# Performance work log

Measured on AMD Instinct MI355X. Metric: run time of the kernel, lower is better.

## Reference

```python
import jax, jax.numpy as jnp
import numpy as np

NEG_INF_FILL = -1000000.0  # matches torch code's masked fill value


def setup_inputs() -> dict:
    key = jax.random.key(0)
    kK, kV, kQ, kL = jax.random.split(key, 4)
    B, Sq, Sk, d, dv = 8, 2048, 2048, 512, 512
    return {
        "K": jax.random.normal(kK, (B, Sk, d), dtype=jnp.float32),
        "V": jax.random.normal(kV, (B, Sk, dv), dtype=jnp.float32),
        "Q": jax.random.normal(kQ, (B, Sq, d), dtype=jnp.float32),
        "valid_len": jax.random.randint(kL, (Sq,), 0, dv, dtype=jnp.int64),
    }


def reference(K, V, Q, valid_len):
    d = K.shape[-1]
    # score: [B, Sq, Sk]
    score = jnp.einsum("bqd,bkd->bqk", Q, K) / jnp.sqrt(jnp.asarray(d, Q.dtype))
    # x: [B, Sq, dv] -- NOTE: original applies mask+softmax to score @ V
    x = jnp.einsum("bqk,bkv->bqv", score, V)
    dv = x.shape[-1]
    # mask rows: per-query-position valid_len compared to feature index 0..dv-1
    mask = jnp.arange(dv)[None, :] > valid_len[:, None]  # [Sq, dv]
    x = jnp.where(mask[None, :, :], jnp.asarray(NEG_INF_FILL, x.dtype), x)
    return jax.nn.softmax(x, axis=-1)
```

## Files before the change

### kernel.cpp

```cpp
#include <hip/hip_runtime.h>
#include <hip/hip_bf16.h>
#include <math.h>

#define BATCH 8
#define SQ 2048
#define SK 2048
#define DD 512
#define DV 512
#define RP 40

typedef short bf16x8_t __attribute__((ext_vector_type(8)));
typedef float f32x4_t __attribute__((ext_vector_type(4)));

__device__ __forceinline__ unsigned int pk_bf16(float a, float b) {
    __hip_bfloat162 h = __float22bfloat162_rn(float2{a, b});
    unsigned int u;
    __builtin_memcpy(&u, &h, 4);
    return u;
}
__device__ __forceinline__ float from_hi(unsigned int u) {
    return __builtin_bit_cast(float, u);
}

__global__ __launch_bounds__(256) void ktv_mfma(const float* __restrict__ Kp,
                                                const float* __restrict__ Vp,
                                                float* __restrict__ Mpart) {
    const int b  = blockIdx.z & 7;
    const int ts = blockIdx.z >> 3;
    const int d0 = blockIdx.x * 128;
    const int v0 = blockIdx.y * 128;
    const float* Kb = Kp + (size_t)b * SK * DD;
    const float* Vb = Vp + (size_t)b * SK * DV;

    __shared__ __align__(16) unsigned short Kh[128 * RP], Kl[128 * RP],
                                            Vh[128 * RP], Vl[128 * RP];

    const int tid  = threadIdx.x;
    const int lane = tid & 63;
    const int w    = tid >> 6;
    const int wd   = (w & 1) * 64;
    const int wv   = (w >> 1) * 64;
    const int uu   = tid >> 5;
    const int xx   = tid & 31;

    f32x4_t acc[4][4];
#pragma unroll
    for (int i = 0; i < 4; ++i)
#pragma unroll
        for (int j = 0; j < 4; ++j) acc[i][j] = (f32x4_t){0.f, 0.f, 0.f, 0.f};

    const int tb = ts * 512;

    float kr0[2][4], kr1[2][4], vr0[2][4], vr1[2][4];
    auto load_tile = [&](int t0l) {
#pragma unroll
        for (int p = 0; p < 2; ++p) {
            const int t = 16 * p + 2 * uu;
            const size_t gr = (size_t)(tb + t0l + t);
#pragma unroll
            for (int c = 0; c < 4; ++c) {
                const int d = xx + 32 * c;
                kr0[p][c] = Kb[gr * DD + d0 + d];
                kr1[p][c] = Kb[(gr + 1) * DD + d0 + d];
                vr0[p][c] = Vb[gr * DV + v0 + d];
                vr1[p][c] = Vb[(gr + 1) * DV + v0 + d];
            }
        }
    };

    load_tile(0);
    for (int t0 = 0; t0 < 512; t0 += 32) {
#pragma unroll
        for (int p = 0; p < 2; ++p) {
            const int t  = 16 * p + 2 * uu;
            const int to = (t >> 3) * 8 + (t & 7);
#pragma unroll
            for (int c = 0; c < 4; ++c) {
                const int d   = xx + 32 * c;
                const int off = d * RP + to;
                {
                    const unsigned int h = pk_bf16(kr0[p][c], kr1[p][c]);
                    const float r0 = kr0[p][c] - from_hi(h << 16);
                    const float r1 = kr1[p][c] - from_hi(h & 0xFFFF0000u);
                    *(unsigned int*)(Kh + off) = h;
                    *(unsigned int*)(Kl + off) = pk_bf16(r0, r1);
                }
                {
                    const unsigned int h = pk_bf16(vr0[p][c], vr1[p][c]);
                    const float r0 = vr0[p][c] - from_hi(h << 16);
                    const float r1 = vr1[p][c] - from_hi(h & 0xFFFF0000u);
                    *(unsigned int*)(Vh + off) = h;
                    *(unsigned int*)(Vl + off) = pk_bf16(r0, r1);
                }
            }
        }
        __syncthreads();

        if (t0 + 32 < 512) load_tile(t0 + 32);

        const int kq = lane >> 4;
        const int mr = lane & 15;
        bf16x8_t ah[4], al_[4];
#pragma unroll
        for (int tm = 0; tm < 4; ++tm) {
            const int off = (wd + tm * 16 + mr) * RP + kq * 8;
            ah[tm]  = *(const bf16x8_t*)(Kh + off);
            al_[tm] = *(const bf16x8_t*)(Kl + off);
        }
#pragma unroll
        for (int tn = 0; tn < 4; ++tn) {
            const int off = (wv + tn * 16 + mr) * RP + kq * 8;
            const bf16x8_t bh = *(const bf16x8_t*)(Vh + off);
            const bf16x8_t bl = *(const bf16x8_t*)(Vl + off);
#pragma unroll
            for (int tm = 0; tm < 4; ++tm) {
                acc[tm][tn] = __builtin_amdgcn_mfma_f32_16x16x32_bf16(ah[tm], bh, acc[tm][tn], 0, 0, 0);
                acc[tm][tn] = __builtin_amdgcn_mfma_f32_16x16x32_bf16(ah[tm], bl, acc[tm][tn], 0, 0, 0);
                acc[tm][tn] = __builtin_amdgcn_mfma_f32_16x16x32_bf16(al_[tm], bh, acc[tm][tn], 0, 0, 0);
            }
        }
        __syncthreads();
    }

    float* Mp = Mpart + (size_t)(ts * 8 + b) * DD * DV;
    const int quad = lane >> 4;
    const int col  = lane & 15;
#pragma unroll
    for (int tm = 0; tm < 4; ++tm)
#pragma unroll
        for (int tn = 0; tn < 4; ++tn)
#pragma unroll
            for (int r = 0; r < 4; ++r) {
                const int d = d0 + wd + tm * 16 + quad * 4 + r;
                const int v = v0 + wv + tn * 16 + col;
                Mp[(size_t)d * DV + v] = acc[tm][tn][r];
            }
}

__global__ __launch_bounds__(256) void reduce_cvt(const float* __restrict__ Mpart,
                                                  unsigned short* __restrict__ Mth,
                                                  unsigned short* __restrict__ Mtl) {
    const int b  = blockIdx.z;
    const int d0 = blockIdx.x * 64;
    const int v0 = blockIdx.y * 64;
    __shared__ float T[64][65];
    const int i  = threadIdx.x;
    const int xr = i >> 4;
    const int xc = i & 15;

#pragma unroll
    for (int e = 0; e < 4; ++e) {
        const int dr = e * 16 + xr;
        float sx = 0.f, sy = 0.f, sz = 0.f, sw = 0.f;
#pragma unroll
        for (int sl = 0; sl < 4; ++sl) {
            const float4 f = *(const float4*)&Mpart[((size_t)(sl * 8 + b) * DD + d0 + dr) * DV + v0 + xc * 4];
            sx += f.x; sy += f.y; sz += f.z; sw += f.w;
        }
        T[dr][xc * 4 + 0] = sx;
        T[dr][xc * 4 + 1] = sy;
        T[dr][xc * 4 + 2] = sz;
        T[dr][xc * 4 + 3] = sw;
    }
    __syncthreads();

    const float s = 0.04419417382415922f;
#pragma unroll
    for (int e = 0; e < 4; ++e) {
        const int v = e * 16 + xr;
        float m[4], r[4];
        unsigned int hv[2], lv[2];
#pragma unroll
        for (int j = 0; j < 4; ++j) m[j] = T[xc * 4 + j][v] * s;
#pragma unroll
        for (int j = 0; j < 2; ++j) {
            hv[j] = pk_bf16(m[2 * j], m[2 * j + 1]);
            r[2 * j]     = m[2 * j]     - from_hi(hv[j] << 16);
            r[2 * j + 1] = m[2 * j + 1] - from_hi(hv[j] & 0xFFFF0000u);
            lv[j] = pk_bf16(r[2 * j], r[2 * j + 1]);
        }
        const size_t o = ((size_t)b * DV + v0 + v) * DD + d0 + xc * 4;
        *(uint2*)&Mth[o] = make_uint2(hv[0], hv[1]);
        *(uint2*)&Mtl[o] = make_uint2(lv[0], lv[1]);
    }
}

__global__ __launch_bounds__(256) void qm_mfma(const float* __restrict__ Qp,
                                               const unsigned short* __restrict__ Mth,
                                               const unsigned short* __restrict__ Mtl,
                                               float* __restrict__ Xp) {
    const int b  = blockIdx.z;
    const int q0 = blockIdx.x * 128;
    const int v0 = blockIdx.y * 128;
    const float* Qb = Qp + (size_t)b * SQ * DD;
    const unsigned short* Bhg = Mth + (size_t)b * DV * DD;
    const unsigned short* Blg = Mtl + (size_t)b * DV * DD;

    __shared__ __align__(16) unsigned short Qh[128 * RP], Ql[128 * RP],
                                            Bh[128 * RP], Bl[128 * RP];

    const int tid  = threadIdx.x;
    const int lane = tid & 63;
    const int w    = tid >> 6;
    const int wq   = (w & 1) * 64;
    const int wv   = (w >> 1) * 64;

    f32x4_t acc[4][4];
#pragma unroll
    for (int i = 0; i < 4; ++i)
#pragma unroll
        for (int j = 0; j < 4; ++j) acc[i][j] = (f32x4_t){0.f, 0.f, 0.f, 0.f};

    float4 pq[4];
    bf16x8_t pbh[2], pbl[2];
    const int qrow = tid >> 3;
    const int qdc  = (tid & 7) * 4;
    const int brow = tid >> 2;
    const int bkq  = tid & 3;
    auto load_tile = [&](int k0l) {
#pragma unroll
        for (int p = 0; p < 4; ++p)
            pq[p] = *(const float4*)&Qb[(size_t)(q0 + p * 32 + qrow) * DD + k0l + qdc];
#pragma unroll
        for (int p = 0; p < 2; ++p) {
            const size_t go = (size_t)(v0 + p * 64 + brow) * DD + k0l + bkq * 8;
            pbh[p] = *(const bf16x8_t*)&Bhg[go];
            pbl[p] = *(const bf16x8_t*)&Blg[go];
        }
    };

    load_tile(0);
    for (int k0 = 0; k0 < DD; k0 += 32) {
#pragma unroll
        for (int p = 0; p < 4; ++p) {
            const float4 f = pq[p];
            const unsigned int h01 = pk_bf16(f.x, f.y);
            const unsigned int h23 = pk_bf16(f.z, f.w);
            const float r0 = f.x - from_hi(h01 << 16);
            const float r1 = f.y - from_hi(h01 & 0xFFFF0000u);
            const float r2 = f.z - from_hi(h23 << 16);
            const float r3 = f.w - from_hi(h23 & 0xFFFF0000u);
            const int off = (p * 32 + qrow) * RP + qdc;
            *(uint2*)(Qh + off) = make_uint2(h01, h23);
            *(uint2*)(Ql + off) = make_uint2(pk_bf16(r0, r1), pk_bf16(r2, r3));
        }
#pragma unroll
        for (int p = 0; p < 2; ++p) {
            const int off = (p * 64 + brow) * RP + bkq * 8;
            *(bf16x8_t*)(Bh + off) = pbh[p];
            *(bf16x8_t*)(Bl + off) = pbl[p];
        }
        __syncthreads();

        if (k0 + 32 < DD) load_tile(k0 + 32);

        const int kq = lane >> 4;
        const int mr = lane & 15;
        bf16x8_t ah[4], al_[4];
#pragma unroll
        for (int tm = 0; tm < 4; ++tm) {
            const int off = (wq + tm * 16 + mr) * RP + kq * 8;
            ah[tm]  = *(const bf16x8_t*)(Qh + off);
            al_[tm] = *(const bf16x8_t*)(Ql + off);
        }
#pragma unroll
        for (int tn = 0; tn < 4; ++tn) {
            const int off = (wv + tn * 16 + mr) * RP + kq * 8;
            const bf16x8_t bh = *(const bf16x8_t*)(Bh + off);
            const bf16x8_t bl = *(const bf16x8_t*)(Bl + off);
#pragma unroll
            for (int tm = 0; tm < 4; ++tm) {
                acc[tm][tn] = __builtin_amdgcn_mfma_f32_16x16x32_bf16(ah[tm], bh, acc[tm][tn], 0, 0, 0);
                acc[tm][tn] = __builtin_amdgcn_mfma_f32_16x16x32_bf16(ah[tm], bl, acc[tm][tn], 0, 0, 0);
                acc[tm][tn] = __builtin_amdgcn_mfma_f32_16x16x32_bf16(al_[tm], bh, acc[tm][tn], 0, 0, 0);
            }
        }
        __syncthreads();
    }

    float* Xb = Xp + (size_t)b * SQ * DV;
    const int quad = lane >> 4;
    const int col  = lane & 15;
#pragma unroll
    for (int tm = 0; tm < 4; ++tm)
#pragma unroll
        for (int tn = 0; tn < 4; ++tn)
#pragma unroll
            for (int r = 0; r < 4; ++r)
                Xb[(size_t)(q0 + wq + tm * 16 + quad * 4 + r) * DV + v0 + wv + tn * 16 + col] = acc[tm][tn][r];
}

__global__ __launch_bounds__(256) void softmax_kernel(float* __restrict__ X,
                                                      const int* __restrict__ vlen) {
    const int wave = threadIdx.x >> 6;
    const int lane = threadIdx.x & 63;
    const int row  = blockIdx.x * 4 + wave;
    const int q    = row & (SQ - 1);
    float* xr = X + (size_t)row * DV;
    const int vl = vlen[q];

    float v[8];
#pragma unroll
    for (int u = 0; u < 2; ++u) {
        const int j0 = u * 256 + lane * 4;
        const float4 f = *(const float4*)&xr[j0];
        v[u * 4 + 0] = (j0 + 0 > vl) ? -1.0e6f : f.x;
        v[u * 4 + 1] = (j0 + 1 > vl) ? -1.0e6f : f.y;
        v[u * 4 + 2] = (j0 + 2 > vl) ? -1.0e6f : f.z;
        v[u * 4 + 3] = (j0 + 3 > vl) ? -1.0e6f : f.w;
    }

    float m = v[0];
#pragma unroll
    for (int i = 1; i < 8; ++i) m = fmaxf(m, v[i]);
#pragma unroll
    for (int off = 32; off > 0; off >>= 1) m = fmaxf(m, __shfl_xor(m, off, 64));

    float ssum = 0.f;
#pragma unroll
    for (int i = 0; i < 8; ++i) {
        v[i] = __expf(v[i] - m);
        ssum += v[i];
    }
#pragma unroll
    for (int off = 32; off > 0; off >>= 1) ssum += __shfl_xor(ssum, off, 64);

    const float inv = 1.0f / ssum;
#pragma unroll
    for (int u = 0; u < 2; ++u) {
        const int j0 = u * 256 + lane * 4;
        float4 o;
        o.x = v[u * 4 + 0] * inv;
        o.y = v[u * 4 + 1] * inv;
        o.z = v[u * 4 + 2] * inv;
        o.w = v[u * 4 + 3] * inv;
        *(float4*)&xr[j0] = o;
    }
}

extern "C" void kernel_launch(void* const* d_in, const int* in_sizes, int n_in,
                              void* d_out, int out_size, void* d_ws, size_t ws_size,
                              hipStream_t stream) {
    const float* Kp   = (const float*)d_in[0];
    const float* Vp   = (const float*)d_in[1];
    const float* Qp   = (const float*)d_in[2];
    const int*   vlen = (const int*)d_in[3];
    float* out = (float*)d_out;

    unsigned short* Mth = (unsigned short*)d_ws;
    unsigned short* Mtl = Mth + (size_t)BATCH * DD * DV;
    float* Mpart = out;

    ktv_mfma<<<dim3(4, 4, 32), 256, 0, stream>>>(Kp, Vp, Mpart);
    reduce_cvt<<<dim3(8, 8, 8), 256, 0, stream>>>(Mpart, Mth, Mtl);
    qm_mfma<<<dim3(16, 4, 8), 256, 0, stream>>>(Qp, Mth, Mtl, out);
    softmax_kernel<<<dim3(BATCH * SQ / 4), 256, 0, stream>>>(out, vlen);
}
```

Measured before the change: 196.2 us.

## Double-buffer register prefetch, vectorize K/V loads, swizzle LDS, raise MFMA priority

Both GEMM kernels now keep two register-staged tiles in flight, so global loads for tile i+2 are issued while tile i is converted and multiplied. The K^T V kernel switches to float4 global loads and an XOR-swizzled LDS layout to cut bank conflicts on the transposed staging writes. Explicit s_barrier, waitcnt, sched_barrier and setprio calls control instruction ordering around the MFMA blocks. In exchange, register pressure rises, which may reduce occupancy.

```diff
diff --git a/kernel.cpp b/kernel.cpp
--- a/kernel.cpp
+++ b/kernel.cpp
@@ -40,8 +40,8 @@
     const int w    = tid >> 6;
     const int wd   = (w & 1) * 64;
     const int wv   = (w >> 1) * 64;
-    const int uu   = tid >> 5;
-    const int xx   = tid & 31;
+    const int tq   = tid >> 5;
+    const int dq   = tid & 31;
 
     f32x4_t acc[4][4];
 #pragma unroll
@@ -50,68 +50,64 @@
         for (int j = 0; j < 4; ++j) acc[i][j] = (f32x4_t){0.f, 0.f, 0.f, 0.f};
 
     const int tb = ts * 512;
-
-    float kr0[2][4], kr1[2][4], vr0[2][4], vr1[2][4];
-    auto load_tile = [&](int t0l) {
-#pragma unroll
-        for (int p = 0; p < 2; ++p) {
-            const int t = 16 * p + 2 * uu;
-            const size_t gr = (size_t)(tb + t0l + t);
-#pragma unroll
-            for (int c = 0; c < 4; ++c) {
-                const int d = xx + 32 * c;
-                kr0[p][c] = Kb[gr * DD + d0 + d];
-                kr1[p][c] = Kb[(gr + 1) * DD + d0 + d];
-                vr0[p][c] = Vb[gr * DV + v0 + d];
-                vr1[p][c] = Vb[(gr + 1) * DV + v0 + d];
+    const int st_col = (8 * tq) ^ (((dq >> 1) & 3) << 4);
+
+    f32x4_t kA[4], vA[4], kB[4], vB[4];
+
+    auto load_t = [&](f32x4_t* kr, f32x4_t* vr, int t0l) {
+#pragma unroll
+        for (int r = 0; r < 4; ++r) {
+            const size_t gr = (size_t)(tb + t0l + 4 * tq + r);
+            kr[r] = *(const f32x4_t*)&Kb[gr * DD + d0 + 4 * dq];
+            vr[r] = *(const f32x4_t*)&Vb[gr * DV + v0 + 4 * dq];
+        }
+    };
+
+    auto stage_t = [&](const f32x4_t* kr, const f32x4_t* vr) {
+#pragma unroll
+        for (int dd = 0; dd < 4; ++dd) {
+            const int boff = (4 * dq + dd) * (2 * RP) + st_col;
+            {
+                const unsigned int h0 = pk_bf16(kr[0][dd], kr[1][dd]);
+                const unsigned int h1 = pk_bf16(kr[2][dd], kr[3][dd]);
+                const float r0 = kr[0][dd] - from_hi(h0 << 16);
+                const float r1 = kr[1][dd] - from_hi(h0 & 0xFFFF0000u);
+                const float r2 = kr[2][dd] - from_hi(h1 << 16);
+                const float r3 = kr[3][dd] - from_hi(h1 & 0xFFFF0000u);
+                *(uint2*)((char*)Kh + boff) = make_uint2(h0, h1);
+                *(uint2*)((char*)Kl + boff) = make_uint2(pk_bf16(r0, r1), pk_bf16(r2, r3));
             }
-        }
-    };
-
-    load_tile(0);
-    for (int t0 = 0; t0 < 512; t0 += 32) {
-#pragma unroll
-        for (int p = 0; p < 2; ++p) {
-            const int t  = 16 * p + 2 * uu;
-            const int to = (t >> 3) * 8 + (t & 7);
-#pragma unroll
-            for (int c = 0; c < 4; ++c) {
-                const int d   = xx + 32 * c;
-                const int off = d * RP + to;
-                {
-                    const unsigned int h = pk_bf16(kr0[p][c], kr1[p][c]);
-                    const float r0 = kr0[p][c] - from_hi(h << 16);
-                    const float r1 = kr1[p][c] - from_hi(h & 0xFFFF0000u);
-                    *(unsigned int*)(Kh + off) = h;
-                    *(unsigned int*)(Kl + off) = pk_bf16(r0, r1);
-                }
-                {
-                    const unsigned int h = pk_bf16(vr0[p][c], vr1[p][c]);
-                    const float r0 = vr0[p][c] - from_hi(h << 16);
-                    const float r1 = vr1[p][c] - from_hi(h & 0xFFFF0000u);
-                    *(unsigned int*)(Vh + off) = h;
-                    *(unsigned int*)(Vl + off) = pk_bf16(r0, r1);
-                }
+            {
+                const unsigned int h0 = pk_bf16(vr[0][dd], vr[1][dd]);
+                const unsigned int h1 = pk_bf16(vr[2][dd], vr[3][dd]);
+                const float r0 = vr[0][dd] - from_hi(h0 << 16);
+                const float r1 = vr[1][dd] - from_hi(h0 & 0xFFFF0000u);
+                const float r2 = vr[2][dd] - from_hi(h1 << 16);
+                const float r3 = vr[3][dd] - from_hi(h1 & 0xFFFF0000u);
+                *(uint2*)((char*)Vh + boff) = make_uint2(h0, h1);
+                *(uint2*)((char*)Vl + boff) = make_uint2(pk_bf16(r0, r1), pk_bf16(r2, r3));
             }
         }
-        __syncthreads();
-
-        if (t0 + 32 < 512) load_tile(t0 + 32);
-
+    };
+
+    auto mfma_block = [&]() {
         const int kq = lane >> 4;
         const int mr = lane & 15;
         bf16x8_t ah[4], al_[4];
 #pragma unroll
         for (int tm = 0; tm < 4; ++tm) {
-            const int off = (wd + tm * 16 + mr) * RP + kq * 8;
-            ah[tm]  = *(const bf16x8_t*)(Kh + off);
-            al_[tm] = *(const bf16x8_t*)(Kl + off);
-        }
+            const int row  = wd + tm * 16 + mr;
+            const int boff = row * (2 * RP) + ((kq * 16) ^ (((row >> 3) & 3) << 4));
+            ah[tm]  = *(const bf16x8_t*)((const char*)Kh + boff);
+            al_[tm] = *(const bf16x8_t*)((const char*)Kl + boff);
+        }
+        __builtin_amdgcn_s_setprio(1);
 #pragma unroll
         for (int tn = 0; tn < 4; ++tn) {
-            const int off = (wv + tn * 16 + mr) * RP + kq * 8;
-            const bf16x8_t bh = *(const bf16x8_t*)(Vh + off);
-            const bf16x8_t bl = *(const bf16x8_t*)(Vl + off);
+            const int row  = wv + tn * 16 + mr;
+            const int boff = row * (2 * RP) + ((kq * 16) ^ (((row >> 3) & 3) << 4));
+            const bf16x8_t bh = *(const bf16x8_t*)((const char*)Vh + boff);
+            const bf16x8_t bl = *(const bf16x8_t*)((const char*)Vl + boff);
 #pragma unroll
             for (int tm = 0; tm < 4; ++tm) {
                 acc[tm][tn] = __builtin_amdgcn_mfma_f32_16x16x32_bf16(ah[tm], bh, acc[tm][tn], 0, 0, 0);
@@ -119,7 +115,34 @@
                 acc[tm][tn] = __builtin_amdgcn_mfma_f32_16x16x32_bf16(al_[tm], bh, acc[tm][tn], 0, 0, 0);
             }
         }
-        __syncthreads();
+        __builtin_amdgcn_s_setprio(0);
+    };
+
+    load_t(kA, vA, 0);
+    load_t(kB, vB, 32);
+
+    for (int t0 = 0; t0 < 512; t0 += 64) {
+        stage_t(kA, vA);
+        asm volatile("s_waitcnt lgkmcnt(0)" ::: "memory");
+        __builtin_amdgcn_s_barrier();
+        __builtin_amdgcn_sched_barrier(0);
+        if (t0 + 64 < 512) load_t(kA, vA, t0 + 64);
+        __builtin_amdgcn_sched_barrier(0);
+        mfma_block();
+        asm volatile("s_waitcnt lgkmcnt(0)" ::: "memory");
+        __builtin_amdgcn_s_barrier();
+        __builtin_amdgcn_sched_barrier(0);
+
+        stage_t(kB, vB);
+        asm volatile("s_waitcnt lgkmcnt(0)" ::: "memory");
+        __builtin_amdgcn_s_barrier();
+        __builtin_amdgcn_sched_barrier(0);
+        if (t0 + 96 < 512) load_t(kB, vB, t0 + 96);
+        __builtin_amdgcn_sched_barrier(0);
+        mfma_block();
+        asm volatile("s_waitcnt lgkmcnt(0)" ::: "memory");
+        __builtin_amdgcn_s_barrier();
+        __builtin_amdgcn_sched_barrier(0);
     }
 
     float* Mp = Mpart + (size_t)(ts * 8 + b) * DD * DV;
@@ -211,16 +234,18 @@
 #pragma unroll
         for (int j = 0; j < 4; ++j) acc[i][j] = (f32x4_t){0.f, 0.f, 0.f, 0.f};
 
-    float4 pq[4];
-    bf16x8_t pbh[2], pbl[2];
     const int qrow = tid >> 3;
     const int qdc  = (tid & 7) * 4;
     const int brow = tid >> 2;
     const int bkq  = tid & 3;
-    auto load_tile = [&](int k0l) {
+
+    f32x4_t  qA[4], qB[4];
+    bf16x8_t bhA[2], blA[2], bhB[2], blB[2];
+
+    auto load_q = [&](f32x4_t* pq, bf16x8_t* pbh, bf16x8_t* pbl, int k0l) {
 #pragma unroll
         for (int p = 0; p < 4; ++p)
-            pq[p] = *(const float4*)&Qb[(size_t)(q0 + p * 32 + qrow) * DD + k0l + qdc];
+            pq[p] = *(const f32x4_t*)&Qb[(size_t)(q0 + p * 32 + qrow) * DD + k0l + qdc];
 #pragma unroll
         for (int p = 0; p < 2; ++p) {
             const size_t go = (size_t)(v0 + p * 64 + brow) * DD + k0l + bkq * 8;
@@ -229,17 +254,16 @@
         }
     };
 
-    load_tile(0);
-    for (int k0 = 0; k0 < DD; k0 += 32) {
+    auto stage_q = [&](const f32x4_t* pq, const bf16x8_t* pbh, const bf16x8_t* pbl) {
 #pragma unroll
         for (int p = 0; p < 4; ++p) {
-            const float4 f = pq[p];
-            const unsigned int h01 = pk_bf16(f.x, f.y);
-            const unsigned int h23 = pk_bf16(f.z, f.w);
-            const float r0 = f.x - from_hi(h01 << 16);
-            const float r1 = f.y - from_hi(h01 & 0xFFFF0000u);
-            const float r2 = f.z - from_hi(h23 << 16);
-            const float r3 = f.w - from_hi(h23 & 0xFFFF0000u);
+            const f32x4_t f = pq[p];
+            const unsigned int h01 = pk_bf16(f[0], f[1]);
+            const unsigned int h23 = pk_bf16(f[2], f[3]);
+            const float r0 = f[0] - from_hi(h01 << 16);
+            const float r1 = f[1] - from_hi(h01 & 0xFFFF0000u);
+            const float r2 = f[2] - from_hi(h23 << 16);
+            const float r3 = f[3] - from_hi(h23 & 0xFFFF0000u);
             const int off = (p * 32 + qrow) * RP + qdc;
             *(uint2*)(Qh + off) = make_uint2(h01, h23);
             *(uint2*)(Ql + off) = make_uint2(pk_bf16(r0, r1), pk_bf16(r2, r3));
@@ -250,10 +274,9 @@
             *(bf16x8_t*)(Bh + off) = pbh[p];
             *(bf16x8_t*)(Bl + off) = pbl[p];
         }
-        __syncthreads();
-
-        if (k0 + 32 < DD) load_tile(k0 + 32);
-
+    };
+
+    auto mfma_block = [&]() {
         const int kq = lane >> 4;
         const int mr = lane & 15;
         bf16x8_t ah[4], al_[4];
@@ -263,6 +286,7 @@
             ah[tm]  = *(const bf16x8_t*)(Qh + off);
             al_[tm] = *(const bf16x8_t*)(Ql + off);
         }
+        __builtin_amdgcn_s_setprio(1);
 #pragma unroll
         for (int tn = 0; tn < 4; ++tn) {
             const int off = (wv + tn * 16 + mr) * RP + kq * 8;
@@ -275,7 +299,34 @@
                 acc[tm][tn] = __builtin_amdgcn_mfma_f32_16x16x32_bf16(al_[tm], bh, acc[tm][tn], 0, 0, 0);
             }
         }
-        __syncthreads();
+        __builtin_amdgcn_s_setprio(0);
+    };
+
+    load_q(qA, bhA, blA, 0);
+    load_q(qB, bhB, blB, 32);
+
+    for (int k0 = 0; k0 < DD; k0 += 64) {
+        stage_q(qA, bhA, blA);
+        asm volatile("s_waitcnt lgkmcnt(0)" ::: "memory");
+        __builtin_amdgcn_s_barrier();
+        __builtin_amdgcn_sched_barrier(0);
+        if (k0 + 64 < DD) load_q(qA, bhA, blA, k0 + 64);
+        __builtin_amdgcn_sched_barrier(0);
+        mfma_block();
+        asm volatile("s_waitcnt lgkmcnt(0)" ::: "memory");
+        __builtin_amdgcn_s_barrier();
+        __builtin_amdgcn_sched_barrier(0);
+
+        stage_q(qB, bhB, blB);
+        asm volatile("s_waitcnt lgkmcnt(0)" ::: "memory");
+        __builtin_amdgcn_s_barrier();
+        __builtin_amdgcn_sched_barrier(0);
+        if (k0 + 96 < DD) load_q(qB, bhB, blB, k0 + 96);
+        __builtin_amdgcn_sched_barrier(0);
+        mfma_block();
+        asm volatile("s_waitcnt lgkmcnt(0)" ::: "memory");
+        __builtin_amdgcn_s_barrier();
+        __builtin_amdgcn_sched_barrier(0);
     }
 
     float* Xb = Xp + (size_t)b * SQ * DV;
```

Result: slower. 242.4 us (+23.6%).

## Load qm_mfma operands directly from global into registers, dropping LDS staging

Applied to the files above, without the earlier changes.

The Q·M GEMM kernel no longer stages Q and the bf16 hi/lo M tiles through shared memory. Each lane now loads its MFMA fragments straight from global memory into registers, using a two-stage register double buffer, and does the fp32-to-bf16 hi/lo split itself. This removes the LDS writes, reads and both __syncthreads per k-step. The cost is redundant global loads: each Q fragment is reloaded by the two waves sharing wq, B is read by the waves sharing wv, and Q is split to bf16 multiple times. The launch bound also asks for 2 blocks per SM, which may limit registers.

```diff
diff --git a/kernel.cpp b/kernel.cpp
--- a/kernel.cpp
+++ b/kernel.cpp
@@ -11,6 +11,7 @@
 
 typedef short bf16x8_t __attribute__((ext_vector_type(8)));
 typedef float f32x4_t __attribute__((ext_vector_type(4)));
+typedef unsigned int u32x4_t __attribute__((ext_vector_type(4)));
 
 __device__ __forceinline__ unsigned int pk_bf16(float a, float b) {
     __hip_bfloat162 h = __float22bfloat162_rn(float2{a, b});
@@ -20,6 +21,26 @@
 }
 __device__ __forceinline__ float from_hi(unsigned int u) {
     return __builtin_bit_cast(float, u);
+}
+
+__device__ __forceinline__ void cvt_split8(const f32x4_t a, const f32x4_t b,
+                                           bf16x8_t& hi, bf16x8_t& lo) {
+    const unsigned int h0 = pk_bf16(a[0], a[1]);
+    const unsigned int h1 = pk_bf16(a[2], a[3]);
+    const unsigned int h2 = pk_bf16(b[0], b[1]);
+    const unsigned int h3 = pk_bf16(b[2], b[3]);
+    const float r0 = a[0] - from_hi(h0 << 16);
+    const float r1 = a[1] - from_hi(h0 & 0xFFFF0000u);
+    const float r2 = a[2] - from_hi(h1 << 16);
+    const float r3 = a[3] - from_hi(h1 & 0xFFFF0000u);
+    const float r4 = b[0] - from_hi(h2 << 16);
+    const float r5 = b[1] - from_hi(h2 & 0xFFFF0000u);
+    const float r6 = b[2] - from_hi(h3 << 16);
+    const float r7 = b[3] - from_hi(h3 & 0xFFFF0000u);
+    const u32x4_t hv = {h0, h1, h2, h3};
+    const u32x4_t lv = {pk_bf16(r0, r1), pk_bf16(r2, r3), pk_bf16(r4, r5), pk_bf16(r6, r7)};
+    hi = __builtin_bit_cast(bf16x8_t, hv);
+    lo = __builtin_bit_cast(bf16x8_t, lv);
 }
 
 __global__ __launch_bounds__(256) void ktv_mfma(const float* __restrict__ Kp,
@@ -185,10 +206,10 @@
     }
 }
 
-__global__ __launch_bounds__(256) void qm_mfma(const float* __restrict__ Qp,
-                                               const unsigned short* __restrict__ Mth,
-                                               const unsigned short* __restrict__ Mtl,
-                                               float* __restrict__ Xp) {
+__global__ __launch_bounds__(256, 2) void qm_mfma(const float* __restrict__ Qp,
+                                                  const unsigned short* __restrict__ Mth,
+                                                  const unsigned short* __restrict__ Mtl,
+                                                  float* __restrict__ Xp) {
     const int b  = blockIdx.z;
     const int q0 = blockIdx.x * 128;
     const int v0 = blockIdx.y * 128;
@@ -196,14 +217,13 @@
     const unsigned short* Bhg = Mth + (size_t)b * DV * DD;
     const unsigned short* Blg = Mtl + (size_t)b * DV * DD;
 
-    __shared__ __align__(16) unsigned short Qh[128 * RP], Ql[128 * RP],
-                                            Bh[128 * RP], Bl[128 * RP];
-
     const int tid  = threadIdx.x;
     const int lane = tid & 63;
     const int w    = tid >> 6;
     const int wq   = (w & 1) * 64;
     const int wv   = (w >> 1) * 64;
+    const int kq   = lane >> 4;
+    const int mr   = lane & 15;
 
     f32x4_t acc[4][4];
 #pragma unroll
@@ -211,71 +231,54 @@
 #pragma unroll
         for (int j = 0; j < 4; ++j) acc[i][j] = (f32x4_t){0.f, 0.f, 0.f, 0.f};
 
-    float4 pq[4];
-    bf16x8_t pbh[2], pbl[2];
-    const int qrow = tid >> 3;
-    const int qdc  = (tid & 7) * 4;
-    const int brow = tid >> 2;
-    const int bkq  = tid & 3;
-    auto load_tile = [&](int k0l) {
-#pragma unroll
-        for (int p = 0; p < 4; ++p)
-            pq[p] = *(const float4*)&Qb[(size_t)(q0 + p * 32 + qrow) * DD + k0l + qdc];
-#pragma unroll
-        for (int p = 0; p < 2; ++p) {
-            const size_t go = (size_t)(v0 + p * 64 + brow) * DD + k0l + bkq * 8;
-            pbh[p] = *(const bf16x8_t*)&Bhg[go];
-            pbl[p] = *(const bf16x8_t*)&Blg[go];
+    const float* qptr[4];
+    size_t boff[4];
+#pragma unroll
+    for (int tm = 0; tm < 4; ++tm)
+        qptr[tm] = Qb + (size_t)(q0 + wq + tm * 16 + mr) * DD + kq * 8;
+#pragma unroll
+    for (int tn = 0; tn < 4; ++tn)
+        boff[tn] = (size_t)(v0 + wv + tn * 16 + mr) * DD + kq * 8;
+
+    f32x4_t  qrA[4][2], qrB[4][2];
+    bf16x8_t bhA[4], blA[4], bhB[4], blB[4];
+
+    auto loadQ = [&](f32x4_t (*qr)[2], int k) {
+#pragma unroll
+        for (int tm = 0; tm < 4; ++tm) {
+            qr[tm][0] = *(const f32x4_t*)(qptr[tm] + k);
+            qr[tm][1] = *(const f32x4_t*)(qptr[tm] + k + 4);
         }
     };
-
-    load_tile(0);
-    for (int k0 = 0; k0 < DD; k0 += 32) {
-#pragma unroll
-        for (int p = 0; p < 4; ++p) {
-            const float4 f = pq[p];
-            const unsigned int h01 = pk_bf16(f.x, f.y);
-            const unsigned int h23 = pk_bf16(f.z, f.w);
-            const float r0 = f.x - from_hi(h01 << 16);
-            const float r1 = f.y - from_hi(h01 & 0xFFFF0000u);
-            const float r2 = f.z - from_hi(h23 << 16);
-            const float r3 = f.w - from_hi(h23 & 0xFFFF0000u);
-            const int off = (p * 32 + qrow) * RP + qdc;
-            *(uint2*)(Qh + off) = make_uint2(h01, h23);
-            *(uint2*)(Ql + off) = make_uint2(pk_bf16(r0, r1), pk_bf16(r2, r3));
-        }
-#pragma unroll
-        for (int p = 0; p < 2; ++p) {
-            const int off = (p * 64 + brow) * RP + bkq * 8;
-            *(bf16x8_t*)(Bh + off) = pbh[p];
-            *(bf16x8_t*)(Bl + off) = pbl[p];
-        }
-        __syncthreads();
-
-        if (k0 + 32 < DD) load_tile(k0 + 32);
-
-        const int kq = lane >> 4;
-        const int mr = lane & 15;
+    auto loadB = [&](bf16x8_t* bh, bf16x8_t* bl, int k) {
+#pragma unroll
+        for (int tn = 0; tn < 4; ++tn) {
+            bh[tn] = *(const bf16x8_t*)&Bhg[boff[tn] + k];
+            bl[tn] = *(const bf16x8_t*)&Blg[boff[tn] + k];
+        }
+    };
+    auto body = [&](f32x4_t (*qr)[2], const bf16x8_t* bh, const bf16x8_t* bl) {
         bf16x8_t ah[4], al_[4];
 #pragma unroll
-        for (int tm = 0; tm < 4; ++tm) {
-            const int off = (wq + tm * 16 + mr) * RP + kq * 8;
-            ah[tm]  = *(const bf16x8_t*)(Qh + off);
-            al_[tm] = *(const bf16x8_t*)(Ql + off);
-        }
-#pragma unroll
-        for (int tn = 0; tn < 4; ++tn) {
-            const int off = (wv + tn * 16 + mr) * RP + kq * 8;
-            const bf16x8_t bh = *(const bf16x8_t*)(Bh + off);
-            const bf16x8_t bl = *(const bf16x8_t*)(Bl + off);
+        for (int tm = 0; tm < 4; ++tm)
+            cvt_split8(qr[tm][0], qr[tm][1], ah[tm], al_[tm]);
+#pragma unroll
+        for (int tn = 0; tn < 4; ++tn)
 #pragma unroll
             for (int tm = 0; tm < 4; ++tm) {
-                acc[tm][tn] = __builtin_amdgcn_mfma_f32_16x16x32_bf16(ah[tm], bh, acc[tm][tn], 0, 0, 0);
-                acc[tm][tn] = __builtin_amdgcn_mfma_f32_16x16x32_bf16(ah[tm], bl, acc[tm][tn], 0, 0, 0);
-                acc[tm][tn] = __builtin_amdgcn_mfma_f32_16x16x32_bf16(al_[tm], bh, acc[tm][tn], 0, 0, 0);
-            }
-        }
-        __syncthreads();
+                acc[tm][tn] = __builtin_amdgcn_mfma_f32_16x16x32_bf16(ah[tm], bh[tn], acc[tm][tn], 0, 0, 0);
+                acc[tm][tn] = __builtin_amdgcn_mfma_f32_16x16x32_bf16(ah[tm], bl[tn], acc[tm][tn], 0, 0, 0);
+                acc[tm][tn] = __builtin_amdgcn_mfma_f32_16x16x32_bf16(al_[tm], bh[tn], acc[tm][tn], 0, 0, 0);
+            }
+    };
+
+    loadQ(qrA, 0);
+    loadB(bhA, blA, 0);
+    for (int k0 = 0; k0 < DD; k0 += 64) {
+        if (k0 + 32 < DD) { loadQ(qrB, k0 + 32); loadB(bhB, blB, k0 + 32); }
+        body(qrA, bhA, blA);
+        if (k0 + 64 < DD) { loadQ(qrA, k0 + 64); loadB(bhA, blA, k0 + 64); }
+        body(qrB, bhB, blB);
     }
 
     float* Xb = Xp + (size_t)b * SQ * DV;
```

Measured after the change: 234.8 us. 19.7% more time.
